# Kernel tuning notes

Measured on AMD Instinct MI355X. Metric: run time of the kernel, lower is better.

The kernel has to match this reference:

```python
import jax, jax.numpy as jnp
import numpy as np

M = 4        # multi_anchor
B = 256      # graphs per batch
NPG = 64     # nodes per graph
N = B * NPG  # total nodes
DEG = 8
E = N * DEG
DF = 16      # raw node feature dim
D = 256      # emb_dim
L = 5        # num_layer
NA = 2       # num_anchor
TASKS = 10
T = 1.0


def _gnn_node(h, edge_src, edge_dst, gin_W1, gin_b1, gin_W2, gin_b2, eps):
    # GIN-style message passing: gather -> sum-scatter -> 2-layer MLP, per layer.
    for l in range(L):
        msg = h[:, edge_src]                                  # [M,E,D] gather
        agg = jnp.zeros_like(h).at[:, edge_dst].add(msg)      # [M,N,D] scatter-add
        z = (1.0 + eps[l]) * h + agg
        z = jax.nn.relu(z @ gin_W1[l] + gin_b1[l])
        h = jax.nn.relu(z @ gin_W2[l] + gin_b2[l])
    return h


def _mindist(h):
    # per-node min squared distance to other nodes in the same graph
    hg = h.reshape(M, B, NPG, D)
    sq = jnp.sum(hg * hg, axis=-1)                            # [M,B,n]
    d2 = sq[..., :, None] + sq[..., None, :] - 2.0 * jnp.einsum('mbid,mbjd->mbij', hg, hg)
    d2 = jnp.maximum(d2, 0.0) + jnp.eye(NPG, dtype=h.dtype) * 1e9
    return jnp.min(d2, axis=-1).reshape(M, N)


def reference(x, W_enc, b_enc, gin_W1, gin_b1, gin_W2, gin_b2, eps,
              anchor_emb, W_n2n, b_n2n, W_pred, b_pred, edge_src, edge_dst):
    # InputEncoder (float x -> MLP with tail activation)
    h0 = jax.nn.relu(x @ W_enc + b_enc)                       # [N,D]
    tx = jnp.broadcast_to(h0[None], (M, N, D))                # expand over multi_anchor
    anchor = jnp.zeros((M, N), dtype=jnp.int32)
    xcur = tx
    skey = jax.random.key(42)
    goff = jnp.arange(B) * NPG                                # graph offsets
    rows = jnp.arange(M)[:, None]
    for i in range(1, NA + 1):
        h = _gnn_node(xcur, edge_src, edge_dst, gin_W1, gin_b1, gin_W2, gin_b2, eps)
        mind = _mindist(h)                                    # [M,N]
        pred = -mind - 10.0 * (anchor > 0).astype(h.dtype)    # mask prior anchors
        logits = (pred * T).reshape(M, B, NPG)
        # categorical sample per (anchor-row, graph) via Gumbel-max == multinomial_sample_batch
        u = jax.random.uniform(jax.random.fold_in(skey, i), (M, B, NPG), minval=1e-9, maxval=1.0)
        idx = jnp.argmax(logits - jnp.log(-jnp.log(u)), axis=-1)  # [M,B]
        glob = idx + goff[None, :]
        anchor = anchor.at[rows, glob].set(i)
        xcur = tx * anchor_emb[anchor] + tx
    h = _gnn_node(xcur, edge_src, edge_dst, gin_W1, gin_b1, gin_W2, gin_b2, eps)
    hn = jax.nn.relu(h @ W_n2n + b_n2n)                       # node2node (tailact)
    hg = hn.reshape(M, B, NPG, D).mean(axis=2)                # mean graph pooling
    out = hg @ W_pred + b_pred                                # pred_lin
    return out.mean(axis=0)                                   # mean over multi_anchor -> [B,TASKS]


def setup_inputs():
    key = jax.random.key(0)
    ks = jax.random.split(key, 12)
    x = jax.random.normal(ks[0], (N, DF), dtype=jnp.float32)
    gid = jnp.repeat(jnp.arange(B), NPG * DEG)
    edge_src = gid * NPG + jax.random.randint(ks[1], (E,), 0, NPG)
    edge_dst = gid * NPG + jax.random.randint(ks[2], (E,), 0, NPG)
    s = lambda k, shp: (jax.random.normal(k, shp, dtype=jnp.float32) * 0.05)
    return {
        'x': x,
        'W_enc': s(ks[3], (DF, D)), 'b_enc': jnp.zeros((D,), jnp.float32),
        'gin_W1': s(ks[4], (L, D, D)), 'gin_b1': jnp.zeros((L, D), jnp.float32),
        'gin_W2': s(ks[5], (L, D, D)), 'gin_b2': jnp.zeros((L, D), jnp.float32),
        'eps': jnp.zeros((L,), jnp.float32),
        'anchor_emb': s(ks[6], (NA + 1, D)),
        'W_n2n': s(ks[7], (D, D)), 'b_n2n': jnp.zeros((D,), jnp.float32),
        'W_pred': s(ks[8], (D, TASKS)), 'b_pred': jnp.zeros((TASKS,), jnp.float32),
        'edge_src': edge_src, 'edge_dst': edge_dst,
    }
```

## Files before the change

kernel.cpp:

```cpp
#include <hip/hip_runtime.h>
#include <stdint.h>

typedef unsigned short u16;
typedef _Float16 f16;
typedef f16 f16x8 __attribute__((ext_vector_type(8)));
typedef float f32x16 __attribute__((ext_vector_type(16)));

#define M_     4
#define B_     256
#define NPG_   64
#define N_     (B_*NPG_)
#define DEG_   8
#define E_     (N_*DEG_)
#define DF_    16
#define D_     256
#define L_     5
#define NA_    2
#define TASKS_ 10

#define HROW 520
#define MFMA16(a,b,c) __builtin_amdgcn_mfma_f32_32x32x16_f16(a,b,c,0,0,0)

__device__ __forceinline__ u16 h_bits(f16 h) { union { f16 h; u16 u; } c; c.h = h; return c.u; }
__device__ __forceinline__ f16 bits_h(u16 u) { union { u16 u; f16 h; } c; c.u = u; return c.h; }
__device__ __forceinline__ float h2f(u16 u) { return (float)bits_h(u); }
__device__ __forceinline__ void split_f16(float v, u16& hi, u16& lo) {
  f16 h = (f16)v;
  f16 l = (f16)(v - (float)h);
  hi = h_bits(h); lo = h_bits(l);
}

__device__ __forceinline__ int haddr8(int row, int chunk) {
  return row * HROW + ((chunk ^ (row & 7)) << 4);
}
__device__ __forceinline__ void write_split(u16* hfU, int row, int col, float v) {
  const int ad = haddr8(row, col >> 3) + (col & 7);
  u16 hi, lo; split_f16(v, hi, lo);
  hfU[ad] = hi; hfU[ad + 8] = lo;
}
__device__ __forceinline__ void write_hi(u16* hfU, int row, int col, float v) {
  const int ad = haddr8(row, col >> 3) + (col & 7);
  hfU[ad] = h_bits((f16)v);
}

__device__ __forceinline__ uint32_t rotl32(uint32_t v, int r) { return (v << r) | (v >> (32 - r)); }
__device__ __forceinline__ void threefry2x32(uint32_t k0, uint32_t k1, uint32_t x0, uint32_t x1,
                                             uint32_t& o0, uint32_t& o1) {
  const uint32_t ks2 = k0 ^ k1 ^ 0x1BD11BDAu;
  x0 += k0; x1 += k1;
#define TFR(r) { x0 += x1; x1 = rotl32(x1, r); x1 ^= x0; }
  TFR(13) TFR(15) TFR(26) TFR(6)   x0 += k1;  x1 += ks2 + 1u;
  TFR(17) TFR(29) TFR(16) TFR(24)  x0 += ks2; x1 += k0 + 2u;
  TFR(13) TFR(15) TFR(26) TFR(6)   x0 += k0;  x1 += k1 + 3u;
  TFR(17) TFR(29) TFR(16) TFR(24)  x0 += k1;  x1 += ks2 + 4u;
  TFR(13) TFR(15) TFR(26) TFR(6)   x0 += ks2; x1 += k0 + 5u;
#undef TFR
  o0 = x0; o1 = x1;
}

template<int TERMS>
__device__ __forceinline__ void gemm_w_mfma(u16* __restrict__ hfU, const u16* __restrict__ WTm,
                                            const float* __restrict__ bias, bool do_relu) {
  const int tid = threadIdx.x;
  const int lane = tid & 63, w = tid >> 6;
  const int l31 = lane & 31, lh = lane >> 5;
  const int col = w * 32 + l31;
  const float bv = bias[col];

  f32x16 acc0 = {}, acc1 = {};
  const u16* Bbase = WTm + col * 8;
#pragma unroll
  for (int ks = 0; ks < 16; ++ks) {
    const int chunk = ks * 2 + lh;
    const int a0 = haddr8(l31, chunk);
    const int a1 = haddr8(32 + l31, chunk);
    const f16x8 ahi0 = *(const f16x8*)(hfU + a0);
    const f16x8 ahi1 = *(const f16x8*)(hfU + a1);
    const f16x8 bh = *(const f16x8*)(Bbase + chunk * 2048);
    if (TERMS == 3) {
      const f16x8 alo0 = *(const f16x8*)(hfU + a0 + 8);
      const f16x8 alo1 = *(const f16x8*)(hfU + a1 + 8);
      const f16x8 bl = *(const f16x8*)(Bbase + chunk * 2048 + 65536);
      acc0 = MFMA16(ahi0, bh, acc0);
      acc0 = MFMA16(ahi0, bl, acc0);
      acc0 = MFMA16(alo0, bh, acc0);
      acc1 = MFMA16(ahi1, bh, acc1);
      acc1 = MFMA16(ahi1, bl, acc1);
      acc1 = MFMA16(alo1, bh, acc1);
    } else {
      acc0 = MFMA16(ahi0, bh, acc0);
      acc1 = MFMA16(ahi1, bh, acc1);
    }
  }
  __syncthreads();
#pragma unroll
  for (int r = 0; r < 16; ++r) {
    const int rr = (r & 3) + 8 * (r >> 2) + 4 * lh;
    float v0 = acc0[r] + bv;
    float v1 = acc1[r] + bv;
    if (do_relu) { v0 = fmaxf(v0, 0.f); v1 = fmaxf(v1, 0.f); }
    if (TERMS == 3) {
      write_split(hfU, rr, col, v0);
      write_split(hfU, 32 + rr, col, v1);
    } else {
      write_hi(hfU, rr, col, v0);
      write_hi(hfU, 32 + rr, col, v1);
    }
  }
  __syncthreads();
}

template<int TERMS>
__device__ __forceinline__ void gemm_adj_mfma(u16* __restrict__ hfU, const u16* __restrict__ AdjU,
                                              float epsl) {
  const int tid = threadIdx.x;
  const int lane = tid & 63, w = tid >> 6;
  const int l31 = lane & 31, lh = lane >> 5;
  const int d = w * 32 + l31;
  const int dc = d >> 3, de = d & 7;
  f32x16 acc0 = {}, acc1 = {};
#pragma unroll
  for (int kk = 0; kk < 4; ++kk) {
    const f16x8 A0 = *(const f16x8*)(AdjU + l31 * 72 + (kk * 2 + lh) * 8);
    const f16x8 A1 = *(const f16x8*)(AdjU + (32 + l31) * 72 + (kk * 2 + lh) * 8);
    const int jb = kk * 16 + lh * 8;
    f16x8 bh, bl;
#pragma unroll
    for (int jj = 0; jj < 8; ++jj) {
      const int j = jb + jj;
      const int ad = haddr8(j, dc) + de;
      bh[jj] = bits_h(hfU[ad]);
      if (TERMS == 3) bl[jj] = bits_h(hfU[ad + 8]);
    }
    acc0 = MFMA16(A0, bh, acc0);
    acc1 = MFMA16(A1, bh, acc1);
    if (TERMS == 3) {
      acc0 = MFMA16(A0, bl, acc0);
      acc1 = MFMA16(A1, bl, acc1);
    }
  }
  float self0[16], self1[16];
#pragma unroll
  for (int r = 0; r < 16; ++r) {
    const int rr = (r & 3) + 8 * (r >> 2) + 4 * lh;
    { const int ad = haddr8(rr, dc) + de;
      self0[r] = (TERMS == 3) ? (h2f(hfU[ad]) + h2f(hfU[ad + 8])) : h2f(hfU[ad]); }
    { const int ad = haddr8(32 + rr, dc) + de;
      self1[r] = (TERMS == 3) ? (h2f(hfU[ad]) + h2f(hfU[ad + 8])) : h2f(hfU[ad]); }
  }
  __syncthreads();
#pragma unroll
  for (int r = 0; r < 16; ++r) {
    const int rr = (r & 3) + 8 * (r >> 2) + 4 * lh;
    if (TERMS == 3) {
      write_split(hfU, rr, d, acc0[r] + epsl * self0[r]);
      write_split(hfU, 32 + rr, d, acc1[r] + epsl * self1[r]);
    } else {
      write_hi(hfU, rr, d, acc0[r] + epsl * self0[r]);
      write_hi(hfU, 32 + rr, d, acc1[r] + epsl * self1[r]);
    }
  }
  __syncthreads();
}

__device__ __forceinline__ void mindist_mfma(u16* __restrict__ hfU, float* __restrict__ mindS) {
  const int tid = threadIdx.x;
  const int lane = tid & 63, w = tid >> 6;
  const int gb = w & 3, gi = gb >> 1, gj = gb & 1, ks = w >> 2;
  const int l31 = lane & 31, lh = lane >> 5;
  f32x16 acc = {};
#pragma unroll
  for (int t = 0; t < 8; ++t) {
    const int chunk = 4 * t + 2 * ks + lh;
    const int ra = haddr8(gi * 32 + l31, chunk);
    const int rb_ = haddr8(gj * 32 + l31, chunk);
    const f16x8 ahi = *(const f16x8*)(hfU + ra);
    const f16x8 alo = *(const f16x8*)(hfU + ra + 8);
    const f16x8 bhi = *(const f16x8*)(hfU + rb_);
    const f16x8 blo = *(const f16x8*)(hfU + rb_ + 8);
    acc = MFMA16(ahi, bhi, acc);
    acc = MFMA16(ahi, blo, acc);
    acc = MFMA16(alo, bhi, acc);
  }
  __syncthreads();
  float* hfF = (float*)hfU;
  if (ks == 1) {
#pragma unroll
    for (int r = 0; r < 16; ++r) {
      const int rr = (r & 3) + 8 * (r >> 2) + 4 * lh;
      hfF[gb * 1088 + rr * 34 + l31] = acc[r];
    }
  }
  __syncthreads();
  if (ks == 0) {
#pragma unroll
    for (int r = 0; r < 16; ++r) {
      const int rr = (r & 3) + 8 * (r >> 2) + 4 * lh;
      const float g = acc[r] + hfF[gb * 1088 + rr * 34 + l31];
      hfF[8192 + (gi * 32 + rr) * 66 + gj * 32 + l31] = g;
    }
  }
  __syncthreads();
  {
    const int i = tid >> 3, jt = tid & 7;
    const float gii = hfF[8192 + i * 66 + i];
    float dmin = 3.4e38f;
#pragma unroll
    for (int jj = 0; jj < 8; ++jj) {
      const int j = jt * 8 + jj;
      const float gjj = hfF[8192 + j * 66 + j];
      const float gij = hfF[8192 + i * 66 + j];
      float d2 = fmaxf(gii + gjj - 2.f * gij, 0.f);
      if (j == i) d2 += 1e9f;
      dmin = fminf(dmin, d2);
    }
    dmin = fminf(dmin, __shfl_xor(dmin, 1));
    dmin = fminf(dmin, __shfl_xor(dmin, 2));
    dmin = fminf(dmin, __shfl_xor(dmin, 4));
    if (jt == 0) mindS[i] = dmin;
  }
  __syncthreads();
}

__device__ __forceinline__ void stage_adj(u16* AdjU, const float* AdjF, int b, int tid) {
  const float* src = AdjF + b * 4096;
  for (int t = tid; t < 4096; t += 512)
    AdjU[(t >> 6) * 72 + (t & 63)] = h_bits((f16)src[t]);
}

template<bool WRITE_LO>
__device__ __forceinline__ void build_xcur(u16* hfU, const float* h0g, const float* aemb,
                                           const int* anchorS, int b, int tid) {
  const int i = tid >> 3, part = tid & 7;
  const float* t = h0g + (b * 64 + i) * 256;
  const float* e = aemb + anchorS[i] * D_;
#pragma unroll
  for (int c = 0; c < 4; ++c) {
    const int chunk = part * 4 + c;
    const float4 tv0 = *(const float4*)(t + chunk * 8);
    const float4 tv1 = *(const float4*)(t + chunk * 8 + 4);
    const float4 ev0 = *(const float4*)(e + chunk * 8);
    const float4 ev1 = *(const float4*)(e + chunk * 8 + 4);
    float vv[8];
    vv[0] = fmaf(tv0.x, ev0.x, tv0.x); vv[1] = fmaf(tv0.y, ev0.y, tv0.y);
    vv[2] = fmaf(tv0.z, ev0.z, tv0.z); vv[3] = fmaf(tv0.w, ev0.w, tv0.w);
    vv[4] = fmaf(tv1.x, ev1.x, tv1.x); vv[5] = fmaf(tv1.y, ev1.y, tv1.y);
    vv[6] = fmaf(tv1.z, ev1.z, tv1.z); vv[7] = fmaf(tv1.w, ev1.w, tv1.w);
    f16x8 hi8, lo8;
#pragma unroll
    for (int ee = 0; ee < 8; ++ee) { u16 h, l; split_f16(vv[ee], h, l); hi8[ee] = bits_h(h); lo8[ee] = bits_h(l); }
    const int a = haddr8(i, chunk);
    *(f16x8*)(hfU + a) = hi8;
    if (WRITE_LO) *(f16x8*)(hfU + a + 8) = lo8;
  }
}

__device__ __forceinline__ void sample_anchor(const float* mindS, float* scoreS, int* anchorS,
                                              int m, int b, int iter, int tid) {
  if (tid < 64) {
    const int j = tid;
    uint32_t k0, k1;
    threefry2x32(0u, 42u, 0u, (uint32_t)iter, k0, k1);
    const uint32_t p = (uint32_t)(m * (B_ * NPG_) + b * NPG_ + j);
    uint32_t o0, o1, bits;
    if (p < 32768u) { threefry2x32(k0, k1, p, p + 32768u, o0, o1); bits = o0; }
    else            { threefry2x32(k0, k1, p - 32768u, p, o0, o1); bits = o1; }
    const float f = __uint_as_float((bits >> 9) | 0x3f800000u) - 1.0f;
    const float uv = fmaxf(1e-9f, f + 1e-9f);
    const float pred = -mindS[j] - ((anchorS[j] > 0) ? 10.0f : 0.0f);
    scoreS[j] = pred - logf(-logf(uv));
  }
  __syncthreads();
  if (tid == 0) {
    int best = 0; float bv = scoreS[0];
    for (int j = 1; j < 64; ++j) { const float v = scoreS[j]; if (v > bv) { bv = v; best = j; } }
    anchorS[best] = iter;
  }
}

__global__ void build_adj_kernel(const int* __restrict__ esrc, const int* __restrict__ edst,
                                 float* __restrict__ AdjF) {
  const int e = blockIdx.x * 256 + threadIdx.x;
  if (e < E_) {
    const int s = esrc[e];
    const int d = edst[e];
    const int g = s >> 6;
    atomicAdd(AdjF + g * 4096 + (d & 63) * 64 + (s & 63), 1.0f);
  }
}

__global__ __launch_bounds__(256) void prep_wt(const float* __restrict__ gW1, const float* __restrict__ gW2,
                                               const float* __restrict__ Wn2n, u16* __restrict__ WTbuf) {
  const int mat = blockIdx.x;
  const float* Wsrc = (mat < 5) ? (gW1 + mat * 65536)
                    : (mat < 10) ? (gW2 + (mat - 5) * 65536) : Wn2n;
  u16* dst = WTbuf + (size_t)mat * 131072;
  const int base = blockIdx.y * 2048;
  for (int idx = base + threadIdx.x; idx < base + 2048; idx += 256) {
    const int k = idx >> 8, d = idx & 255;
    const float a = Wsrc[idx];
    u16 hi, lo; split_f16(a, hi, lo);
    const int off = (k >> 3) * 2048 + d * 8 + (k & 7);
    dst[off] = hi;
    dst[65536 + off] = lo;
  }
}

__global__ __launch_bounds__(512)
void gnn1_kernel(const float* __restrict__ x, const float* __restrict__ Wenc,
                 const float* __restrict__ benc, float* __restrict__ h0g,
                 const float* __restrict__ AdjF, const u16* __restrict__ WTbuf,
                 const float* __restrict__ gb1, const float* __restrict__ gb2,
                 const float* __restrict__ eps, float* __restrict__ mindG) {
  __shared__ __align__(16) u16 hfU[64 * HROW];
  __shared__ __align__(16) u16 AdjU[64 * 72];
  __shared__ float mindS[64];
  const int tid = threadIdx.x;
  const int b = blockIdx.x;

  {
    float* scr = (float*)hfU;
    for (int t = tid; t < 4096; t += 512) {
      const int k = t >> 8, d = t & 255;
      scr[k * 264 + d + (d >> 5)] = Wenc[t];
    }
    if (tid < 256) scr[4300 + tid] = benc[tid];
    for (int t = tid; t < 1024; t += 512) scr[4600 + t] = x[b * 1024 + t];
    __syncthreads();

    const int i = tid >> 3, part = tid & 7;
    float xv[16];
#pragma unroll
    for (int k = 0; k < 16; ++k) xv[k] = scr[4600 + i * 16 + k];
    float hv[32];
#pragma unroll
    for (int dd = 0; dd < 32; ++dd) {
      const int d = part * 32 + dd;
      float acc = scr[4300 + d];
#pragma unroll
      for (int k = 0; k < 16; ++k) acc = fmaf(xv[k], scr[k * 264 + d + (d >> 5)], acc);
      hv[dd] = fmaxf(acc, 0.f);
    }
    float* dst = h0g + (b * 64 + i) * 256 + part * 32;
#pragma unroll
    for (int dd = 0; dd < 32; dd += 4) {
      float4 v; v.x = hv[dd]; v.y = hv[dd + 1]; v.z = hv[dd + 2]; v.w = hv[dd + 3];
      *(float4*)(dst + dd) = v;
    }
    __syncthreads();
#pragma unroll
    for (int c = 0; c < 4; ++c) {
      f16x8 hi8, lo8;
#pragma unroll
      for (int e = 0; e < 8; ++e) { u16 h, l; split_f16(hv[c * 8 + e], h, l); hi8[e] = bits_h(h); lo8[e] = bits_h(l); }
      const int a = haddr8(i, part * 4 + c);
      *(f16x8*)(hfU + a) = hi8;
      *(f16x8*)(hfU + a + 8) = lo8;
    }
  }
  stage_adj(AdjU, AdjF, b, tid);
  __syncthreads();

  for (int l = 0; l < L_; ++l) {
    const float epsl = 1.0f + eps[l];
    gemm_adj_mfma<3>(hfU, AdjU, epsl);
    gemm_w_mfma<3>(hfU, WTbuf + (size_t)l * 131072,       gb1 + l * D_, true);
    gemm_w_mfma<3>(hfU, WTbuf + (size_t)(5 + l) * 131072, gb2 + l * D_, true);
  }
  mindist_mfma(hfU, mindS);
  if (tid < 64) mindG[b * 64 + tid] = mindS[tid];
}

__global__ __launch_bounds__(512, 4)
void mega_kernel(const float* __restrict__ h0g, const float* __restrict__ AdjF,
                 const u16* __restrict__ WTbuf,
                 const float* __restrict__ gb1, const float* __restrict__ gb2,
                 const float* __restrict__ eps, const float* __restrict__ aemb,
                 const float* __restrict__ bn2n,
                 const float* __restrict__ Wpred, const float* __restrict__ bpred,
                 const float* __restrict__ mindG, float* __restrict__ outp) {
  __shared__ __align__(16) u16 hfU[64 * HROW];
  __shared__ __align__(16) u16 AdjU[64 * 72];
  __shared__ float mindS[64];
  __shared__ float scoreS[64];
  __shared__ float hgS[256];
  __shared__ int   anchorS[64];

  const int tid = threadIdx.x;
  const int b = blockIdx.x;
  const int m = blockIdx.y;

  stage_adj(AdjU, AdjF, b, tid);
  if (tid < 64) { anchorS[tid] = 0; mindS[tid] = mindG[b * 64 + tid]; }
  __syncthreads();

  sample_anchor(mindS, scoreS, anchorS, m, b, 1, tid);
  __syncthreads();
  build_xcur<true>(hfU, h0g, aemb, anchorS, b, tid);
  __syncthreads();

  for (int l = 0; l < L_; ++l) {
    const float epsl = 1.0f + eps[l];
    gemm_adj_mfma<3>(hfU, AdjU, epsl);
    gemm_w_mfma<3>(hfU, WTbuf + (size_t)l * 131072,       gb1 + l * D_, true);
    gemm_w_mfma<3>(hfU, WTbuf + (size_t)(5 + l) * 131072, gb2 + l * D_, true);
  }
  mindist_mfma(hfU, mindS);
  sample_anchor(mindS, scoreS, anchorS, m, b, 2, tid);
  __syncthreads();
  build_xcur<false>(hfU, h0g, aemb, anchorS, b, tid);
  __syncthreads();

  for (int l = 0; l < L_; ++l) {
    const float epsl = 1.0f + eps[l];
    gemm_adj_mfma<1>(hfU, AdjU, epsl);
    gemm_w_mfma<1>(hfU, WTbuf + (size_t)l * 131072,       gb1 + l * D_, true);
    gemm_w_mfma<1>(hfU, WTbuf + (size_t)(5 + l) * 131072, gb2 + l * D_, true);
  }

  gemm_w_mfma<1>(hfU, WTbuf + (size_t)10 * 131072, bn2n, true);
  if (tid < 256) {
    const int dc = tid >> 3, de = tid & 7;
    float s = 0.f;
    for (int i = 0; i < 64; ++i)
      s += h2f(hfU[haddr8(i, dc) + de]);
    hgS[tid] = s * (1.0f / 64.0f);
  }
  __syncthreads();
  if (tid < 160) {
    const int t = tid >> 4, part = tid & 15;
    float s = 0.f;
    for (int d = part * 16; d < part * 16 + 16; ++d) s = fmaf(hgS[d], Wpred[d * TASKS_ + t], s);
    s += __shfl_xor(s, 1); s += __shfl_xor(s, 2); s += __shfl_xor(s, 4); s += __shfl_xor(s, 8);
    if (part == 0) {
      float val = s * 0.25f;
      if (m == 0) val += bpred[t];
      atomicAdd(outp + b * TASKS_ + t, val);
    }
  }
}

extern "C" void kernel_launch(void* const* d_in, const int* in_sizes, int n_in,
                              void* d_out, int out_size, void* d_ws, size_t ws_size,
                              hipStream_t stream) {
  const float* x     = (const float*)d_in[0];
  const float* Wenc  = (const float*)d_in[1];
  const float* benc  = (const float*)d_in[2];
  const float* gW1   = (const float*)d_in[3];
  const float* gb1   = (const float*)d_in[4];
  const float* gW2   = (const float*)d_in[5];
  const float* gb2   = (const float*)d_in[6];
  const float* eps   = (const float*)d_in[7];
  const float* aemb  = (const float*)d_in[8];
  const float* Wn2n  = (const float*)d_in[9];
  const float* bn2n  = (const float*)d_in[10];
  const float* Wpred = (const float*)d_in[11];
  const float* bpred = (const float*)d_in[12];
  const int* esrc    = (const int*)d_in[13];
  const int* edst    = (const int*)d_in[14];
  float* outp = (float*)d_out;

  float* h0g  = (float*)d_ws;
  float* AdjF = h0g + (size_t)N_ * D_;
  u16* WTbuf  = (u16*)(AdjF + B_ * 4096);
  float* mindG = (float*)(WTbuf + (size_t)11 * 131072);

  hipMemsetAsync(AdjF, 0, (size_t)B_ * 4096 * sizeof(float), stream);
  hipMemsetAsync(outp, 0, (size_t)out_size * sizeof(float), stream);
  build_adj_kernel<<<dim3((E_ + 255) / 256), dim3(256), 0, stream>>>(esrc, edst, AdjF);
  prep_wt<<<dim3(11, 32), dim3(256), 0, stream>>>(gW1, gW2, Wn2n, WTbuf);
  gnn1_kernel<<<dim3(B_), dim3(512), 0, stream>>>(x, Wenc, benc, h0g, AdjF, WTbuf,
                                                  gb1, gb2, eps, mindG);
  mega_kernel<<<dim3(B_, M_), dim3(512), 0, stream>>>(h0g, AdjF, WTbuf, gb1, gb2,
                                                      eps, aemb, bn2n, Wpred, bpred, mindG, outp);
}
```

Measured before the change: 679.0 us.

## Reorder GIN layer as (A+eps I)(hW1) with transposed intermediate layout

Uses associativity to compute h@W1 first, writing the result transposed, and then applies the adjacency (with 1+eps folded onto its diagonal) as an MFMA with vectorized operand loads. This replaces the scalar gather of B operands and the separate self-term reads in the old adjacency GEMM. Outputs are now written as packed f16x4 stores instead of scalar u16 writes. A fallback path corrects the diagonal when diag+1+eps is not exactly representable in f16, and the shared buffer grows to hold the 256x64 transposed tile.

```diff
diff --git a/kernel.cpp b/kernel.cpp
--- a/kernel.cpp
+++ b/kernel.cpp
@@ -3,6 +3,7 @@
 
 typedef unsigned short u16;
 typedef _Float16 f16;
+typedef f16 f16x4 __attribute__((ext_vector_type(4)));
 typedef f16 f16x8 __attribute__((ext_vector_type(8)));
 typedef float f32x16 __attribute__((ext_vector_type(16)));
 
@@ -19,6 +20,7 @@
 #define TASKS_ 10
 
 #define HROW 520
+#define TROW 136
 #define MFMA16(a,b,c) __builtin_amdgcn_mfma_f32_32x32x16_f16(a,b,c,0,0,0)
 
 __device__ __forceinline__ u16 h_bits(f16 h) { union { f16 h; u16 u; } c; c.h = h; return c.u; }
@@ -33,14 +35,8 @@
 __device__ __forceinline__ int haddr8(int row, int chunk) {
   return row * HROW + ((chunk ^ (row & 7)) << 4);
 }
-__device__ __forceinline__ void write_split(u16* hfU, int row, int col, float v) {
-  const int ad = haddr8(row, col >> 3) + (col & 7);
-  u16 hi, lo; split_f16(v, hi, lo);
-  hfU[ad] = hi; hfU[ad + 8] = lo;
-}
-__device__ __forceinline__ void write_hi(u16* hfU, int row, int col, float v) {
-  const int ad = haddr8(row, col >> 3) + (col & 7);
-  hfU[ad] = h_bits((f16)v);
+__device__ __forceinline__ int taddr8(int d, int c) {
+  return d * TROW + ((c ^ (d & 7)) << 4);
 }
 
 __device__ __forceinline__ uint32_t rotl32(uint32_t v, int r) { return (v << r) | (v >> (32 - r)); }
@@ -59,14 +55,13 @@
 }
 
 template<int TERMS>
-__device__ __forceinline__ void gemm_w_mfma(u16* __restrict__ hfU, const u16* __restrict__ WTm,
-                                            const float* __restrict__ bias, bool do_relu) {
+__device__ __forceinline__ void gemm_w_RT(u16* __restrict__ hfU, const u16* __restrict__ WTm,
+                                          const float* __restrict__ bias, bool do_relu) {
   const int tid = threadIdx.x;
   const int lane = tid & 63, w = tid >> 6;
   const int l31 = lane & 31, lh = lane >> 5;
   const int col = w * 32 + l31;
-  const float bv = bias[col];
-
+  const float bv = bias ? bias[col] : 0.f;
   f32x16 acc0 = {}, acc1 = {};
   const u16* Bbase = WTm + col * 8;
 #pragma unroll
@@ -94,71 +89,155 @@
   }
   __syncthreads();
 #pragma unroll
-  for (int r = 0; r < 16; ++r) {
-    const int rr = (r & 3) + 8 * (r >> 2) + 4 * lh;
-    float v0 = acc0[r] + bv;
-    float v1 = acc1[r] + bv;
-    if (do_relu) { v0 = fmaxf(v0, 0.f); v1 = fmaxf(v1, 0.f); }
-    if (TERMS == 3) {
-      write_split(hfU, rr, col, v0);
-      write_split(hfU, 32 + rr, col, v1);
-    } else {
-      write_hi(hfU, rr, col, v0);
-      write_hi(hfU, 32 + rr, col, v1);
-    }
+  for (int q = 0; q < 4; ++q) {
+    f16x4 h4a, l4a, h4b, l4b;
+#pragma unroll
+    for (int e = 0; e < 4; ++e) {
+      float v0 = acc0[q * 4 + e] + bv;
+      float v1 = acc1[q * 4 + e] + bv;
+      if (do_relu) { v0 = fmaxf(v0, 0.f); v1 = fmaxf(v1, 0.f); }
+      if (TERMS == 3) {
+        u16 hi, lo;
+        split_f16(v0, hi, lo); h4a[e] = bits_h(hi); l4a[e] = bits_h(lo);
+        split_f16(v1, hi, lo); h4b[e] = bits_h(hi); l4b[e] = bits_h(lo);
+      } else {
+        h4a[e] = (f16)v0; h4b[e] = (f16)v1;
+      }
+    }
+    const int t0 = taddr8(col, q) + 4 * lh;
+    const int t1 = taddr8(col, 4 + q) + 4 * lh;
+    *(f16x4*)(hfU + t0) = h4a;
+    *(f16x4*)(hfU + t1) = h4b;
+    if (TERMS == 3) { *(f16x4*)(hfU + t0 + 8) = l4a; *(f16x4*)(hfU + t1 + 8) = l4b; }
   }
   __syncthreads();
 }
 
 template<int TERMS>
-__device__ __forceinline__ void gemm_adj_mfma(u16* __restrict__ hfU, const u16* __restrict__ AdjU,
-                                              float epsl) {
+__device__ __forceinline__ void gemm_adj_TR(u16* __restrict__ hfU, const u16* __restrict__ AdjU,
+                                            const float* __restrict__ bias, int slow,
+                                            const float* __restrict__ diagC, float epsl) {
   const int tid = threadIdx.x;
   const int lane = tid & 63, w = tid >> 6;
   const int l31 = lane & 31, lh = lane >> 5;
-  const int d = w * 32 + l31;
-  const int dc = d >> 3, de = d & 7;
+  const int drow = w * 32 + l31;
   f32x16 acc0 = {}, acc1 = {};
 #pragma unroll
   for (int kk = 0; kk < 4; ++kk) {
-    const f16x8 A0 = *(const f16x8*)(AdjU + l31 * 72 + (kk * 2 + lh) * 8);
-    const f16x8 A1 = *(const f16x8*)(AdjU + (32 + l31) * 72 + (kk * 2 + lh) * 8);
-    const int jb = kk * 16 + lh * 8;
-    f16x8 bh, bl;
-#pragma unroll
-    for (int jj = 0; jj < 8; ++jj) {
-      const int j = jb + jj;
-      const int ad = haddr8(j, dc) + de;
-      bh[jj] = bits_h(hfU[ad]);
-      if (TERMS == 3) bl[jj] = bits_h(hfU[ad + 8]);
-    }
-    acc0 = MFMA16(A0, bh, acc0);
-    acc1 = MFMA16(A1, bh, acc1);
+    const int chunk = kk * 2 + lh;
+    const int ta = taddr8(drow, chunk);
+    const f16x8 uh = *(const f16x8*)(hfU + ta);
+    const f16x8 B0 = *(const f16x8*)(AdjU + l31 * 72 + chunk * 8);
+    const f16x8 B1 = *(const f16x8*)(AdjU + (32 + l31) * 72 + chunk * 8);
+    acc0 = MFMA16(uh, B0, acc0);
+    acc1 = MFMA16(uh, B1, acc1);
     if (TERMS == 3) {
-      acc0 = MFMA16(A0, bl, acc0);
-      acc1 = MFMA16(A1, bl, acc1);
-    }
-  }
-  float self0[16], self1[16];
-#pragma unroll
-  for (int r = 0; r < 16; ++r) {
-    const int rr = (r & 3) + 8 * (r >> 2) + 4 * lh;
-    { const int ad = haddr8(rr, dc) + de;
-      self0[r] = (TERMS == 3) ? (h2f(hfU[ad]) + h2f(hfU[ad + 8])) : h2f(hfU[ad]); }
-    { const int ad = haddr8(32 + rr, dc) + de;
-      self1[r] = (TERMS == 3) ? (h2f(hfU[ad]) + h2f(hfU[ad + 8])) : h2f(hfU[ad]); }
-  }
-  __syncthreads();
-#pragma unroll
-  for (int r = 0; r < 16; ++r) {
-    const int rr = (r & 3) + 8 * (r >> 2) + 4 * lh;
+      const f16x8 ul = *(const f16x8*)(hfU + ta + 8);
+      acc0 = MFMA16(ul, B0, acc0);
+      acc1 = MFMA16(ul, B1, acc1);
+    }
+  }
+  if (slow) {
+    const int i0 = l31, i1 = 32 + l31;
+    const float v0d = diagC[i0] + epsl, v1d = diagC[i1] + epsl;
+    const float r0 = v0d - h2f(h_bits((f16)v0d));
+    const float r1 = v1d - h2f(h_bits((f16)v1d));
+#pragma unroll
+    for (int r = 0; r < 16; ++r) {
+      const int dp = w * 32 + (r & 3) + 8 * (r >> 2) + 4 * lh;
+      const int a0 = taddr8(dp, i0 >> 3) + (i0 & 7);
+      const int a1 = taddr8(dp, i1 >> 3) + (i1 & 7);
+      float u0 = h2f(hfU[a0]);
+      float u1 = h2f(hfU[a1]);
+      if (TERMS == 3) { u0 += h2f(hfU[a0 + 8]); u1 += h2f(hfU[a1 + 8]); }
+      acc0[r] += r0 * u0;
+      acc1[r] += r1 * u1;
+    }
+  }
+  __syncthreads();
+#pragma unroll
+  for (int q = 0; q < 4; ++q) {
+    f16x4 h4a, l4a, h4b, l4b;
+#pragma unroll
+    for (int e = 0; e < 4; ++e) {
+      const int r = q * 4 + e;
+      const float bq = bias[w * 32 + 8 * q + 4 * lh + e];
+      float v0 = fmaxf(acc0[r] + bq, 0.f);
+      float v1 = fmaxf(acc1[r] + bq, 0.f);
+      if (TERMS == 3) {
+        u16 hi, lo;
+        split_f16(v0, hi, lo); h4a[e] = bits_h(hi); l4a[e] = bits_h(lo);
+        split_f16(v1, hi, lo); h4b[e] = bits_h(hi); l4b[e] = bits_h(lo);
+      } else {
+        h4a[e] = (f16)v0; h4b[e] = (f16)v1;
+      }
+    }
+    const int c = w * 4 + q;
+    const int a0 = haddr8(l31, c) + 4 * lh;
+    const int a1 = haddr8(32 + l31, c) + 4 * lh;
+    *(f16x4*)(hfU + a0) = h4a;
+    *(f16x4*)(hfU + a1) = h4b;
+    if (TERMS == 3) { *(f16x4*)(hfU + a0 + 8) = l4a; *(f16x4*)(hfU + a1 + 8) = l4b; }
+  }
+  __syncthreads();
+}
+
+template<int TERMS>
+__device__ __forceinline__ void gemm_w_RR(u16* __restrict__ hfU, const u16* __restrict__ WTm,
+                                          const float* __restrict__ bias, bool do_relu) {
+  const int tid = threadIdx.x;
+  const int lane = tid & 63, w = tid >> 6;
+  const int l31 = lane & 31, lh = lane >> 5;
+  f32x16 acc0 = {}, acc1 = {};
+  const u16* Abase = WTm + (w * 32 + l31) * 8;
+#pragma unroll
+  for (int ks = 0; ks < 16; ++ks) {
+    const int chunk = ks * 2 + lh;
+    const f16x8 Wh = *(const f16x8*)(Abase + chunk * 2048);
+    const int b0 = haddr8(l31, chunk);
+    const int b1_ = haddr8(32 + l31, chunk);
+    const f16x8 Xh0 = *(const f16x8*)(hfU + b0);
+    const f16x8 Xh1 = *(const f16x8*)(hfU + b1_);
     if (TERMS == 3) {
-      write_split(hfU, rr, d, acc0[r] + epsl * self0[r]);
-      write_split(hfU, 32 + rr, d, acc1[r] + epsl * self1[r]);
+      const f16x8 Wl = *(const f16x8*)(Abase + chunk * 2048 + 65536);
+      const f16x8 Xl0 = *(const f16x8*)(hfU + b0 + 8);
+      const f16x8 Xl1 = *(const f16x8*)(hfU + b1_ + 8);
+      acc0 = MFMA16(Wh, Xh0, acc0);
+      acc0 = MFMA16(Wl, Xh0, acc0);
+      acc0 = MFMA16(Wh, Xl0, acc0);
+      acc1 = MFMA16(Wh, Xh1, acc1);
+      acc1 = MFMA16(Wl, Xh1, acc1);
+      acc1 = MFMA16(Wh, Xl1, acc1);
     } else {
-      write_hi(hfU, rr, d, acc0[r] + epsl * self0[r]);
-      write_hi(hfU, 32 + rr, d, acc1[r] + epsl * self1[r]);
-    }
+      acc0 = MFMA16(Wh, Xh0, acc0);
+      acc1 = MFMA16(Wh, Xh1, acc1);
+    }
+  }
+  __syncthreads();
+#pragma unroll
+  for (int q = 0; q < 4; ++q) {
+    f16x4 h4a, l4a, h4b, l4b;
+#pragma unroll
+    for (int e = 0; e < 4; ++e) {
+      const int r = q * 4 + e;
+      const float bq = bias[w * 32 + 8 * q + 4 * lh + e];
+      float v0 = acc0[r] + bq;
+      float v1 = acc1[r] + bq;
+      if (do_relu) { v0 = fmaxf(v0, 0.f); v1 = fmaxf(v1, 0.f); }
+      if (TERMS == 3) {
+        u16 hi, lo;
+        split_f16(v0, hi, lo); h4a[e] = bits_h(hi); l4a[e] = bits_h(lo);
+        split_f16(v1, hi, lo); h4b[e] = bits_h(hi); l4b[e] = bits_h(lo);
+      } else {
+        h4a[e] = (f16)v0; h4b[e] = (f16)v1;
+      }
+    }
+    const int c = w * 4 + q;
+    const int a0 = haddr8(l31, c) + 4 * lh;
+    const int a1 = haddr8(32 + l31, c) + 4 * lh;
+    *(f16x4*)(hfU + a0) = h4a;
+    *(f16x4*)(hfU + a1) = h4b;
+    if (TERMS == 3) { *(f16x4*)(hfU + a0 + 8) = l4a; *(f16x4*)(hfU + a1 + 8) = l4b; }
   }
   __syncthreads();
 }
@@ -312,9 +391,11 @@
                  const float* __restrict__ AdjF, const u16* __restrict__ WTbuf,
                  const float* __restrict__ gb1, const float* __restrict__ gb2,
                  const float* __restrict__ eps, float* __restrict__ mindG) {
-  __shared__ __align__(16) u16 hfU[64 * HROW];
+  __shared__ __align__(16) u16 hfU[256 * TROW];
   __shared__ __align__(16) u16 AdjU[64 * 72];
   __shared__ float mindS[64];
+  __shared__ float diagC[64];
+  __shared__ int flagS;
   const int tid = threadIdx.x;
   const int b = blockIdx.x;
 
@@ -359,13 +440,26 @@
     }
   }
   stage_adj(AdjU, AdjF, b, tid);
-  __syncthreads();
+  if (tid == 0) flagS = 0;
+  if (tid < 64) {
+    const float dc = AdjF[b * 4096 + tid * 65];
+    diagC[tid] = dc;
+    int f = 0;
+    for (int l = 0; l < L_; ++l) {
+      const float v = dc + 1.0f + eps[l];
+      if (h2f(h_bits((f16)v)) != v) f = 1;
+    }
+    if (f) atomicOr(&flagS, 1);
+  }
+  __syncthreads();
+  const int slow = flagS;
 
   for (int l = 0; l < L_; ++l) {
     const float epsl = 1.0f + eps[l];
-    gemm_adj_mfma<3>(hfU, AdjU, epsl);
-    gemm_w_mfma<3>(hfU, WTbuf + (size_t)l * 131072,       gb1 + l * D_, true);
-    gemm_w_mfma<3>(hfU, WTbuf + (size_t)(5 + l) * 131072, gb2 + l * D_, true);
+    if (tid < 64) AdjU[tid * 72 + tid] = h_bits((f16)(diagC[tid] + epsl));
+    gemm_w_RT<3>(hfU, WTbuf + (size_t)l * 131072, nullptr, false);
+    gemm_adj_TR<3>(hfU, AdjU, gb1 + l * D_, slow, diagC, epsl);
+    gemm_w_RR<3>(hfU, WTbuf + (size_t)(5 + l) * 131072, gb2 + l * D_, true);
   }
   mindist_mfma(hfU, mindS);
   if (tid < 64) mindG[b * 64 + tid] = mindS[tid];
@@ -379,31 +473,48 @@
                  const float* __restrict__ bn2n,
                  const float* __restrict__ Wpred, const float* __restrict__ bpred,
                  const float* __restrict__ mindG, float* __restrict__ outp) {
-  __shared__ __align__(16) u16 hfU[64 * HROW];
+  __shared__ __align__(16) u16 hfU[256 * TROW];
   __shared__ __align__(16) u16 AdjU[64 * 72];
   __shared__ float mindS[64];
   __shared__ float scoreS[64];
   __shared__ float hgS[256];
   __shared__ int   anchorS[64];
+  __shared__ float diagC[64];
+  __shared__ int   flagS;
 
   const int tid = threadIdx.x;
   const int b = blockIdx.x;
   const int m = blockIdx.y;
 
   stage_adj(AdjU, AdjF, b, tid);
-  if (tid < 64) { anchorS[tid] = 0; mindS[tid] = mindG[b * 64 + tid]; }
+  if (tid == 0) flagS = 0;
+  if (tid < 64) {
+    anchorS[tid] = 0;
+    mindS[tid] = mindG[b * 64 + tid];
+    const float dc = AdjF[b * 4096 + tid * 65];
+    diagC[tid] = dc;
+    int f = 0;
+    for (int l = 0; l < L_; ++l) {
+      const float v = dc + 1.0f + eps[l];
+      if (h2f(h_bits((f16)v)) != v) f = 1;
+    }
+    if (f) atomicOr(&flagS, 1);
+  }
   __syncthreads();
 
   sample_anchor(mindS, scoreS, anchorS, m, b, 1, tid);
   __syncthreads();
   build_xcur<true>(hfU, h0g, aemb, anchorS, b, tid);
   __syncthreads();
+
+  const int slow = flagS;
 
   for (int l = 0; l < L_; ++l) {
     const float epsl = 1.0f + eps[l];
-    gemm_adj_mfma<3>(hfU, AdjU, epsl);
-    gemm_w_mfma<3>(hfU, WTbuf + (size_t)l * 131072,       gb1 + l * D_, true);
-    gemm_w_mfma<3>(hfU, WTbuf + (size_t)(5 + l) * 131072, gb2 + l * D_, true);
+    if (tid < 64) AdjU[tid * 72 + tid] = h_bits((f16)(diagC[tid] + epsl));
+    gemm_w_RT<3>(hfU, WTbuf + (size_t)l * 131072, nullptr, false);
+    gemm_adj_TR<3>(hfU, AdjU, gb1 + l * D_, slow, diagC, epsl);
+    gemm_w_RR<3>(hfU, WTbuf + (size_t)(5 + l) * 131072, gb2 + l * D_, true);
   }
   mindist_mfma(hfU, mindS);
   sample_anchor(mindS, scoreS, anchorS, m, b, 2, tid);
@@ -413,17 +524,21 @@
 
   for (int l = 0; l < L_; ++l) {
     const float epsl = 1.0f + eps[l];
-    gemm_adj_mfma<1>(hfU, AdjU, epsl);
-    gemm_w_mfma<1>(hfU, WTbuf + (size_t)l * 131072,       gb1 + l * D_, true);
-    gemm_w_mfma<1>(hfU, WTbuf + (size_t)(5 + l) * 131072, gb2 + l * D_, true);
-  }
-
-  gemm_w_mfma<1>(hfU, WTbuf + (size_t)10 * 131072, bn2n, true);
+    if (tid < 64) AdjU[tid * 72 + tid] = h_bits((f16)(diagC[tid] + epsl));
+    gemm_w_RT<1>(hfU, WTbuf + (size_t)l * 131072, nullptr, false);
+    gemm_adj_TR<1>(hfU, AdjU, gb1 + l * D_, slow, diagC, epsl);
+    gemm_w_RR<1>(hfU, WTbuf + (size_t)(5 + l) * 131072, gb2 + l * D_, true);
+  }
+
+  gemm_w_RT<1>(hfU, WTbuf + (size_t)10 * 131072, bn2n, true);
   if (tid < 256) {
-    const int dc = tid >> 3, de = tid & 7;
     float s = 0.f;
-    for (int i = 0; i < 64; ++i)
-      s += h2f(hfU[haddr8(i, dc) + de]);
+#pragma unroll
+    for (int c = 0; c < 8; ++c) {
+      const f16x8 v = *(const f16x8*)(hfU + taddr8(tid, c));
+      s += (float)v[0] + (float)v[1] + (float)v[2] + (float)v[3]
+         + (float)v[4] + (float)v[5] + (float)v[6] + (float)v[7];
+    }
     hgS[tid] = s * (1.0f / 64.0f);
   }
   __syncthreads();
```

New measurement: 679.9 us. No clear change (+0.1%).
